# Performance work log

Hardware: AMD Instinct MI355X
Metric: run time of the kernel (lower is better)

## Reference

```python
import jax, jax.numpy as jnp
import numpy as np

LATENT_DIM = 256
BOOK_SIZE = 8192


def setup_inputs() -> dict:
    key = jax.random.key(0)
    k1, k2 = jax.random.split(key)
    z_e = jax.random.normal(k1, (16, LATENT_DIM, 32, 32), dtype=jnp.float32)
    codebook = jax.random.normal(k2, (BOOK_SIZE, LATENT_DIM), dtype=jnp.float32)
    return {"z_e": z_e, "codebook": codebook}


def reference(z_e, codebook):
    # NCHW -> NHWC -> (B*H*W, D)
    flat_z = jnp.transpose(z_e, (0, 2, 3, 1)).reshape(-1, LATENT_DIM)
    # squared euclidean distance via matmul: ||z||^2 + ||e||^2 - 2 z.e
    dist = (
        jnp.sum(flat_z ** 2, axis=1, keepdims=True)
        + jnp.sum(codebook ** 2, axis=1)
        - 2.0 * flat_z @ codebook.T
    )  # (N, book_size)
    indices = jnp.argmin(dist, axis=1)          # (N,)
    z_q = codebook[indices]                      # (N, D) gather
    return z_q, indices
```

## Files before the change

### kernel.cpp

```cpp
#include <hip/hip_runtime.h>
#include <stdint.h>

#define NROWS 16384
#define NCODES 8192
#define DIM 256
#define EPS_S 0.4f
#define SM 0.8f

typedef __attribute__((ext_vector_type(8))) short bf16x8;
typedef __attribute__((ext_vector_type(16))) float f32x16;
typedef unsigned int uint32;

__device__ __forceinline__ unsigned short f2bf(float f) {
  union { float f; unsigned int u; } v; v.f = f;
  unsigned int u = v.u;
  return (unsigned short)((u + 0x7FFFu + ((u >> 16) & 1u)) >> 16);
}

__device__ __forceinline__ void glds16(const void* g, void* l) {
  __builtin_amdgcn_global_load_lds(
      (const __attribute__((address_space(1))) unsigned int*)g,
      (__attribute__((address_space(3))) unsigned int*)l, 16, 0, 0);
}

__device__ __forceinline__ unsigned long long packdi(float d, int idx) {
  unsigned int u = __float_as_uint(d);
  u = (u & 0x80000000u) ? ~u : (u | 0x80000000u);
  return ((unsigned long long)u << 32) | (unsigned int)idx;
}
__device__ __forceinline__ unsigned long long u64min(unsigned long long a,
                                                     unsigned long long b) {
  return a < b ? a : b;
}
__device__ __forceinline__ unsigned long long shflx64(unsigned long long v, int m) {
  int lo = __shfl_xor((int)(unsigned int)v, m);
  int hi = __shfl_xor((int)(v >> 32), m);
  return ((unsigned long long)(unsigned int)hi << 32) | (unsigned int)lo;
}
__device__ __forceinline__ uint32 umax(uint32 a, uint32 b) { return a > b ? a : b; }
__device__ __forceinline__ uint32 umin(uint32 a, uint32 b) { return a < b ? a : b; }

__global__ __launch_bounds__(256) void prep(const float* __restrict__ z,
                                            const float* __restrict__ cb,
                                            float* __restrict__ flatz,
                                            ushort* __restrict__ zb,
                                            ushort* __restrict__ eb,
                                            float* __restrict__ enorm) {
  __shared__ float t[32][33];
  const int blk = blockIdx.x;
  if (blk < 4096) {
    const int tx = threadIdx.x & 31, ty = threadIdx.x >> 5;
    const int ht = blk & 31, ct = (blk >> 5) & 7, b = blk >> 8;
    const float* src = z + (size_t)b * 262144 + (size_t)(ct * 32) * 1024 + ht * 32;
#pragma unroll
    for (int i = 0; i < 4; ++i) {
      int c = ty + i * 8;
      t[c][tx] = src[c * 1024 + tx];
    }
    __syncthreads();
#pragma unroll
    for (int i = 0; i < 4; ++i) {
      int hw = ty + i * 8;
      int row = b * 1024 + ht * 32 + hw;
      float v = t[tx][hw];
      flatz[(size_t)row * 256 + ct * 32 + tx] = v;
      zb[(size_t)row * 256 + ct * 32 + tx] = f2bf(v);
    }
  } else {
    const int lane = threadIdx.x & 63, wave = threadIdx.x >> 6;
    const int code = (blk - 4096) * 4 + wave;
    float4 v = *(const float4*)(cb + (size_t)code * 256 + lane * 4);
    ushort4 o;
    o.x = f2bf(v.x); o.y = f2bf(v.y); o.z = f2bf(v.z); o.w = f2bf(v.w);
    *(ushort4*)(eb + (size_t)code * 256 + lane * 4) = o;
    float ss = v.x * v.x + v.y * v.y + v.z * v.z + v.w * v.w;
#pragma unroll
    for (int s = 1; s < 64; s <<= 1) ss += __shfl_xor(ss, s);
    if (lane == 0) enorm[code] = ss;
  }
}

__global__ __launch_bounds__(256) void vq_gemm(const ushort* __restrict__ eb,
                                               const ushort* __restrict__ zb,
                                               const float* __restrict__ enorm,
                                               uint32* __restrict__ bm) {
  __shared__ __align__(16) ushort As[2][4096];
  __shared__ __align__(16) ushort Bs[2][4096];
  const int tid = threadIdx.x;
  const int wave = tid >> 6, lane = tid & 63;
  const int wr = wave >> 1, wc = wave & 1;
  const int code0 = blockIdx.x * 128;
  const int zrow0 = blockIdx.y * 128;
  const int l31 = lane & 31, lg = lane >> 5;

  f32x16 acc[2][2];
#pragma unroll
  for (int i = 0; i < 2; ++i) {
    const float* ep = enorm + code0 + wr * 64 + i * 32 + 4 * lg;
    float4 e0 = *(const float4*)(ep);
    float4 e1 = *(const float4*)(ep + 8);
    float4 e2 = *(const float4*)(ep + 16);
    float4 e3 = *(const float4*)(ep + 24);
    f32x16 c0;
    c0[0]  = 1024.f - 0.5f * e0.x; c0[1]  = 1024.f - 0.5f * e0.y;
    c0[2]  = 1024.f - 0.5f * e0.z; c0[3]  = 1024.f - 0.5f * e0.w;
    c0[4]  = 1024.f - 0.5f * e1.x; c0[5]  = 1024.f - 0.5f * e1.y;
    c0[6]  = 1024.f - 0.5f * e1.z; c0[7]  = 1024.f - 0.5f * e1.w;
    c0[8]  = 1024.f - 0.5f * e2.x; c0[9]  = 1024.f - 0.5f * e2.y;
    c0[10] = 1024.f - 0.5f * e2.z; c0[11] = 1024.f - 0.5f * e2.w;
    c0[12] = 1024.f - 0.5f * e3.x; c0[13] = 1024.f - 0.5f * e3.y;
    c0[14] = 1024.f - 0.5f * e3.z; c0[15] = 1024.f - 0.5f * e3.w;
    acc[i][0] = c0; acc[i][1] = c0;
  }

  const int r_in = lane >> 2;
  const int kc = (lane & 3) ^ ((lane >> 3) & 3);
  const ushort* aG0 = eb + (size_t)(code0 + wave * 16 + r_in) * 256 + kc * 8;
  const ushort* aG1 = eb + (size_t)(code0 + 64 + wave * 16 + r_in) * 256 + kc * 8;
  const ushort* bG0 = zb + (size_t)(zrow0 + wave * 16 + r_in) * 256 + kc * 8;
  const ushort* bG1 = zb + (size_t)(zrow0 + 64 + wave * 16 + r_in) * 256 + kc * 8;

  glds16(aG0, &As[0][wave * 512]);
  glds16(aG1, &As[0][(wave + 4) * 512]);
  glds16(bG0, &Bs[0][wave * 512]);
  glds16(bG1, &Bs[0][(wave + 4) * 512]);

  const int ra = wr * 64 + l31;
  const int rb = wc * 64 + l31;
  const int hash = (l31 >> 1) & 3;

#pragma unroll
  for (int k0 = 0; k0 < 8; ++k0) {
    const int cur = k0 & 1;
    __syncthreads();
    if (k0 < 7) {
      glds16(aG0 + (k0 + 1) * 32, &As[cur ^ 1][wave * 512]);
      glds16(aG1 + (k0 + 1) * 32, &As[cur ^ 1][(wave + 4) * 512]);
      glds16(bG0 + (k0 + 1) * 32, &Bs[cur ^ 1][wave * 512]);
      glds16(bG1 + (k0 + 1) * 32, &Bs[cur ^ 1][(wave + 4) * 512]);
    }
    bf16x8 af[2][2], bf[2][2];
#pragma unroll
    for (int i = 0; i < 2; ++i)
#pragma unroll
      for (int h = 0; h < 2; ++h) {
        int slot = (h * 2 + lg) ^ hash;
        af[i][h] = *(const bf16x8*)(&As[cur][(ra + i * 32) * 32 + slot * 8]);
        bf[i][h] = *(const bf16x8*)(&Bs[cur][(rb + i * 32) * 32 + slot * 8]);
      }
#pragma unroll
    for (int h = 0; h < 2; ++h)
#pragma unroll
      for (int i = 0; i < 2; ++i)
#pragma unroll
        for (int j = 0; j < 2; ++j)
          acc[i][j] = __builtin_amdgcn_mfma_f32_32x32x16_bf16(
              af[i][h], bf[j][h], acc[i][j], 0, 0, 0);
  }

  const int cid0 = blockIdx.x * 8 + wr * 4;
#pragma unroll
  for (int j = 0; j < 2; ++j) {
    uint32 res[4];
#pragma unroll
    for (int i = 0; i < 2; ++i)
#pragma unroll
      for (int hc = 0; hc < 2; ++hc) {
        uint32 m1 = 0, m2 = 0;
#pragma unroll
        for (int p = 0; p < 8; ++p) {
          uint32 id = (uint32)((p & 3) | (lg << 2) | ((p >> 2) << 3));
          uint32 pv = (__float_as_uint(acc[i][j][hc * 8 + p]) & ~31u) | id;
          m2 = umax(m2, umin(m1, pv));
          m1 = umax(m1, pv);
        }
        uint32 o1 = (uint32)__shfl_xor((int)m1, 32);
        uint32 o2 = (uint32)__shfl_xor((int)m2, 32);
        m2 = umax(umax(m2, o2), umin(m1, o1));
        m1 = umax(m1, o1);
        float s1 = __uint_as_float(m1 & ~31u);
        float s2 = __uint_as_float(m2 & ~31u);
        res[i * 2 + hc] = (s1 - s2 > SM) ? (m1 | 16u) : m1;
      }
    if (lane < 32) {
      int zr = zrow0 + wc * 64 + j * 32 + l31;
      uint4 o; o.x = res[0]; o.y = res[1]; o.z = res[2]; o.w = res[3];
      *(uint4*)(bm + (size_t)zr * 512 + cid0) = o;
    }
  }
}

__device__ __forceinline__ unsigned long long chunk_exact(
    int chunk, const float* __restrict__ zrow, const float* __restrict__ cb,
    const float* __restrict__ enorm, int lane) {
  const int code = chunk * 16 + (lane >> 2);
  const float* zp = zrow + (lane & 3) * 64;
  const float* cp = cb + (size_t)code * 256 + (lane & 3) * 64;
  float s = 0.f;
#pragma unroll
  for (int d = 0; d < 64; d += 4) {
    float4 zv = *(const float4*)(zp + d);
    float4 cv = *(const float4*)(cp + d);
    s = fmaf(zv.x, cv.x, s); s = fmaf(zv.y, cv.y, s);
    s = fmaf(zv.z, cv.z, s); s = fmaf(zv.w, cv.w, s);
  }
  s += __shfl_xor(s, 1);
  s += __shfl_xor(s, 2);
  float dist = fmaf(-2.f, s, enorm[code]);
  unsigned long long key = ((lane & 3) == 0) ? packdi(dist, code) : ~0ull;
#pragma unroll
  for (int m = 1; m < 64; m <<= 1) key = u64min(key, shflx64(key, m));
  return key;
}

__global__ __launch_bounds__(256) void vq_sel(const uint32* __restrict__ bm,
                                              const float* __restrict__ flatz,
                                              const float* __restrict__ cb,
                                              const float* __restrict__ enorm,
                                              float* __restrict__ zq,
                                              float* __restrict__ oidx) {
  const int lane = threadIdx.x & 63;
  const int row = blockIdx.x * 4 + (threadIdx.x >> 6);
  uint4 va = *(const uint4*)(bm + (size_t)row * 512 + lane * 8);
  uint4 vb = *(const uint4*)(bm + (size_t)row * 512 + lane * 8 + 4);
  uint32 v[8] = {va.x, va.y, va.z, va.w, vb.x, vb.y, vb.z, vb.w};
  uint32 m1 = 0, m2 = 0; int ch = 0;
#pragma unroll
  for (int s = 0; s < 8; ++s) {
    uint32 pv = v[s];
    m2 = umax(m2, umin(m1, pv));
    ch = (pv > m1) ? (lane * 8 + s) : ch;
    m1 = umax(m1, pv);
  }
#pragma unroll
  for (int m = 1; m < 64; m <<= 1) {
    uint32 o1 = (uint32)__shfl_xor((int)m1, m);
    uint32 o2 = (uint32)__shfl_xor((int)m2, m);
    int oc = __shfl_xor(ch, m);
    m2 = umax(umax(m2, o2), umin(m1, o1));
    ch = (o1 > m1) ? oc : ch;
    m1 = umax(m1, o1);
  }
  float s1 = __uint_as_float(m1 & ~31u);
  float s2 = __uint_as_float(m2 & ~31u);
  int idx;
  if ((m1 & 16u) && (s1 - s2 > SM)) {
    idx = ch * 16 + (int)(m1 & 15u);
  } else {
    const float* zrow = flatz + (size_t)row * 256;
    unsigned long long key = chunk_exact(ch, zrow, cb, enorm, lane);
    float dbest;
    { unsigned int u = (unsigned int)(key >> 32);
      u = (u & 0x80000000u) ? (u & 0x7FFFFFFFu) : ~u;
      dbest = __uint_as_float(u); }
    float thr = (1024.f - 0.5f * dbest) - EPS_S;
#pragma unroll
    for (int s = 0; s < 8; ++s) {
      bool cand = __uint_as_float(v[s] & ~31u) >= thr;
      unsigned long long mk = __ballot(cand);
      while (mk) {
        int L = __ffsll(mk) - 1;
        mk &= mk - 1;
        int c2 = L * 8 + s;
        if (c2 == ch) continue;
        key = u64min(key, chunk_exact(c2, zrow, cb, enorm, lane));
      }
    }
    idx = (int)(key & 0xFFFFFFFFull);
  }
  if (lane == 0) oidx[row] = (float)idx;
  float4 val = *(const float4*)(cb + (size_t)idx * 256 + lane * 4);
  *(float4*)(zq + (size_t)row * 256 + lane * 4) = val;
}

extern "C" void kernel_launch(void* const* d_in, const int* in_sizes, int n_in,
                              void* d_out, int out_size, void* d_ws, size_t ws_size,
                              hipStream_t stream) {
  const float* z = (const float*)d_in[0];
  const float* cb = (const float*)d_in[1];
  char* ws = (char*)d_ws;
  ushort* zb = (ushort*)(ws);
  ushort* eb = (ushort*)(ws + (8u << 20));
  float* enorm = (float*)(ws + (12u << 20));
  uint32* bm = (uint32*)(ws + (13u << 20));
  float* zq = (float*)d_out;
  float* oidx = zq + (size_t)NROWS * DIM;
  float* flatz = zq;

  prep<<<4096 + NCODES / 4, 256, 0, stream>>>(z, cb, flatz, zb, eb, enorm);
  vq_gemm<<<dim3(NCODES / 128, NROWS / 128), 256, 0, stream>>>(eb, zb, enorm, bm);
  vq_sel<<<NROWS / 4, 256, 0, stream>>>(bm, flatz, cb, enorm, zq, oidx);
}
```

Measured before the change: 198.6 us.

## Replace direct global-to-LDS loads with register-staged two-deep prefetch pipeline

Swaps the global_load_lds DMA path for ordinary global loads into registers that are written to LDS one step later, keeping two K-steps in flight. The barrier moves to the end of each iteration. The aim is to hide global latency behind the MFMA work with a deeper prefetch. In exchange it uses more VGPRs, adds explicit LDS store instructions, and issues redundant clamped loads in the last iterations.

Measured after the change: 193.1 us. 2.8% less time.

```diff
diff --git a/kernel.cpp b/kernel.cpp
--- a/kernel.cpp
+++ b/kernel.cpp
@@ -15,12 +15,6 @@
   union { float f; unsigned int u; } v; v.f = f;
   unsigned int u = v.u;
   return (unsigned short)((u + 0x7FFFu + ((u >> 16) & 1u)) >> 16);
-}
-
-__device__ __forceinline__ void glds16(const void* g, void* l) {
-  __builtin_amdgcn_global_load_lds(
-      (const __attribute__((address_space(1))) unsigned int*)g,
-      (__attribute__((address_space(3))) unsigned int*)l, 16, 0, 0);
 }
 
 __device__ __forceinline__ unsigned long long packdi(float d, int idx) {
@@ -119,11 +113,19 @@
   const ushort* aG1 = eb + (size_t)(code0 + 64 + wave * 16 + r_in) * 256 + kc * 8;
   const ushort* bG0 = zb + (size_t)(zrow0 + wave * 16 + r_in) * 256 + kc * 8;
   const ushort* bG1 = zb + (size_t)(zrow0 + 64 + wave * 16 + r_in) * 256 + kc * 8;
-
-  glds16(aG0, &As[0][wave * 512]);
-  glds16(aG1, &As[0][(wave + 4) * 512]);
-  glds16(bG0, &Bs[0][wave * 512]);
-  glds16(bG1, &Bs[0][(wave + 4) * 512]);
+  const int wo0 = wave * 512 + lane * 8;
+  const int wo1 = (wave + 4) * 512 + lane * 8;
+
+  bf16x8 pa[2], pb[2], na[2], nb[2];
+  pa[0] = *(const bf16x8*)(aG0);        pa[1] = *(const bf16x8*)(aG1);
+  pb[0] = *(const bf16x8*)(bG0);        pb[1] = *(const bf16x8*)(bG1);
+  na[0] = *(const bf16x8*)(aG0 + 32);   na[1] = *(const bf16x8*)(aG1 + 32);
+  nb[0] = *(const bf16x8*)(bG0 + 32);   nb[1] = *(const bf16x8*)(bG1 + 32);
+  *(bf16x8*)(&As[0][wo0]) = pa[0];
+  *(bf16x8*)(&As[0][wo1]) = pa[1];
+  *(bf16x8*)(&Bs[0][wo0]) = pb[0];
+  *(bf16x8*)(&Bs[0][wo1]) = pb[1];
+  __syncthreads();
 
   const int ra = wr * 64 + l31;
   const int rb = wc * 64 + l31;
@@ -132,12 +134,16 @@
 #pragma unroll
   for (int k0 = 0; k0 < 8; ++k0) {
     const int cur = k0 & 1;
-    __syncthreads();
+    const int kn = (k0 + 2 <= 7) ? (k0 + 2) : 7;
+    bf16x8 qa0 = *(const bf16x8*)(aG0 + kn * 32);
+    bf16x8 qa1 = *(const bf16x8*)(aG1 + kn * 32);
+    bf16x8 qb0 = *(const bf16x8*)(bG0 + kn * 32);
+    bf16x8 qb1 = *(const bf16x8*)(bG1 + kn * 32);
     if (k0 < 7) {
-      glds16(aG0 + (k0 + 1) * 32, &As[cur ^ 1][wave * 512]);
-      glds16(aG1 + (k0 + 1) * 32, &As[cur ^ 1][(wave + 4) * 512]);
-      glds16(bG0 + (k0 + 1) * 32, &Bs[cur ^ 1][wave * 512]);
-      glds16(bG1 + (k0 + 1) * 32, &Bs[cur ^ 1][(wave + 4) * 512]);
+      *(bf16x8*)(&As[cur ^ 1][wo0]) = na[0];
+      *(bf16x8*)(&As[cur ^ 1][wo1]) = na[1];
+      *(bf16x8*)(&Bs[cur ^ 1][wo0]) = nb[0];
+      *(bf16x8*)(&Bs[cur ^ 1][wo1]) = nb[1];
     }
     bf16x8 af[2][2], bf[2][2];
 #pragma unroll
@@ -156,6 +162,8 @@
         for (int j = 0; j < 2; ++j)
           acc[i][j] = __builtin_amdgcn_mfma_f32_32x32x16_bf16(
               af[i][h], bf[j][h], acc[i][j], 0, 0, 0);
+    na[0] = qa0; na[1] = qa1; nb[0] = qb0; nb[1] = qb1;
+    __syncthreads();
   }
 
   const int cid0 = blockIdx.x * 8 + wr * 4;
```
